# Kernel tuning notes

Measured on AMD Instinct MI355X. Metric: run time of the kernel, lower is better.

Reference implementation:

```python
import jax, jax.numpy as jnp
import numpy as np

N = 4096      # nodes
IN = 512      # in_features
HEADS = 8
HPH = 8       # n_hidden // n_heads
HID = HEADS * HPH  # 64
CLS = 16      # n_classes
NEG_SLOPE = 0.2
MASK_VAL = -1e9


def setup_inputs() -> dict:
    key = jax.random.key(0)
    ks = jax.random.split(key, 8)
    x = jax.random.normal(ks[0], (N, IN), jnp.float32)
    # sparse-ish adjacency, avg degree ~16, with self loops
    adj = jax.random.bernoulli(ks[1], 16.0 / N, (N, N)) | jnp.eye(N, dtype=bool)
    W1 = jax.random.normal(ks[2], (IN, HEADS, HPH), jnp.float32) * 0.05
    a1l = jax.random.normal(ks[3], (HEADS, HPH), jnp.float32) * 0.05
    a1r = jax.random.normal(ks[4], (HEADS, HPH), jnp.float32) * 0.05
    W2 = jax.random.normal(ks[5], (HID, 1, CLS), jnp.float32) * 0.05
    a2l = jax.random.normal(ks[6], (1, CLS), jnp.float32) * 0.05
    a2r = jax.random.normal(ks[7], (1, CLS), jnp.float32) * 0.05
    return {"x": x, "adj": adj, "W1": W1, "a1l": a1l, "a1r": a1r,
            "W2": W2, "a2l": a2l, "a2r": a2r}


def gat_layer(x, adj, W, al, ar, is_concat):
    # project: [N, H, D]
    g = jnp.einsum('ni,ihd->nhd', x, W)
    # score e[i,j,h] = leaky_relu(a_l . g_i + a_r . g_j)
    sl = jnp.einsum('nhd,hd->nh', g, al)  # [N, H]
    sr = jnp.einsum('nhd,hd->nh', g, ar)  # [N, H]
    e = jax.nn.leaky_relu(sl[:, None, :] + sr[None, :, :], NEG_SLOPE)  # [N, N, H]
    e = jnp.where(adj[:, :, None], e, MASK_VAL)
    a = jax.nn.softmax(e, axis=1)                 # softmax over neighbors j
    out = jnp.einsum('ijh,jhd->ihd', a, g)        # [N, H, D]
    if is_concat:
        return out.reshape(out.shape[0], -1)      # [N, H*D]
    return out.mean(axis=1)                        # [N, D]


def reference(x, adj, W1, a1l, a1r, W2, a2l, a2r):
    # dropout layers are identity in eval mode
    h = gat_layer(x, adj, W1, a1l, a1r, True)   # [N, HID]
    h = jax.nn.elu(h)
    return gat_layer(h, adj, W2, a2l, a2r, False)  # [N, CLS]
```

## Files before the change

kernel.cpp:

```cpp
#include <hip/hip_runtime.h>
#include <hip/hip_bf16.h>

#define N_NODES 4096
#define IN_F 512
#define HEADS 8
#define HPH 8
#define HID 64
#define CLS 16
#define NEG_SLOPE 0.2f
#define MAXD 256

__device__ __forceinline__ float leaky(float x) { return x > 0.f ? x : NEG_SLOPE * x; }

__global__ void proj1(const float* __restrict__ x,
                      const float* __restrict__ W1,
                      const float* __restrict__ a1l,
                      const float* __restrict__ a1r,
                      float* __restrict__ g1,
                      float* __restrict__ sl1,
                      float* __restrict__ sr1) {
    const int t  = threadIdx.x;
    const int nl = t >> 4;
    const int c4 = (t & 15) * 4;
    const int i0 = blockIdx.x * 16;
    __shared__ float xs[16][516];
    {
        const int row = nl;
        const float4* src = (const float4*)(x + (size_t)(i0 + row) * IN_F);
        float4* dst = (float4*)(&xs[row][0]);
        for (int k = (t & 15); k < IN_F / 4; k += 16) dst[k] = src[k];
    }
    __syncthreads();
    float4 acc = make_float4(0.f, 0.f, 0.f, 0.f);
    const float* xrow = &xs[nl][0];
#pragma unroll 4
    for (int k = 0; k < IN_F; k += 4) {
        const float4 xv = *(const float4*)(xrow + k);
        const float4 w0 = *(const float4*)(W1 + (size_t)(k + 0) * HID + c4);
        const float4 w1 = *(const float4*)(W1 + (size_t)(k + 1) * HID + c4);
        const float4 w2 = *(const float4*)(W1 + (size_t)(k + 2) * HID + c4);
        const float4 w3 = *(const float4*)(W1 + (size_t)(k + 3) * HID + c4);
        acc.x += xv.x * w0.x + xv.y * w1.x + xv.z * w2.x + xv.w * w3.x;
        acc.y += xv.x * w0.y + xv.y * w1.y + xv.z * w2.y + xv.w * w3.y;
        acc.z += xv.x * w0.z + xv.y * w1.z + xv.z * w2.z + xv.w * w3.z;
        acc.w += xv.x * w0.w + xv.y * w1.w + xv.z * w2.w + xv.w * w3.w;
    }
    const int i = i0 + nl;
    *(float4*)(g1 + (size_t)i * HID + c4) = acc;
    const float4 al = *(const float4*)(a1l + c4);
    const float4 ar = *(const float4*)(a1r + c4);
    float pl = acc.x * al.x + acc.y * al.y + acc.z * al.z + acc.w * al.w;
    float pr = acc.x * ar.x + acc.y * ar.y + acc.z * ar.z + acc.w * ar.w;
    pl += __shfl_xor(pl, 1, 64);
    pr += __shfl_xor(pr, 1, 64);
    if ((t & 1) == 0) {
        const int h = (t & 15) >> 1;
        sl1[i * HEADS + h] = pl;
        sr1[i * HEADS + h] = pr;
    }
}

__global__ void attn1_fused(const int* __restrict__ adj,
                            const float* __restrict__ g1,
                            const float* __restrict__ sl1,
                            const float* __restrict__ sr1,
                            const float* __restrict__ W2,
                            const float* __restrict__ a2l,
                            const float* __restrict__ a2r,
                            float* __restrict__ g2,
                            float* __restrict__ sl2,
                            float* __restrict__ sr2,
                            int* __restrict__ deg_g,
                            int* __restrict__ nbr_g) {
    const int i = blockIdx.x;
    const int t = threadIdx.x;
    __shared__ int nbr[MAXD];
    __shared__ int cnt;
    __shared__ float h1s[HID];
    if (t == 0) cnt = 0;
    __syncthreads();
    const int4* row = (const int4*)(adj + (size_t)i * N_NODES);
    for (int w = t; w < N_NODES / 4; w += 64) {
        int4 v = row[w];
        if (v.x | v.y | v.z | v.w) {
            if (v.x) { int p = atomicAdd(&cnt, 1); if (p < MAXD) nbr[p] = 4 * w + 0; }
            if (v.y) { int p = atomicAdd(&cnt, 1); if (p < MAXD) nbr[p] = 4 * w + 1; }
            if (v.z) { int p = atomicAdd(&cnt, 1); if (p < MAXD) nbr[p] = 4 * w + 2; }
            if (v.w) { int p = atomicAdd(&cnt, 1); if (p < MAXD) nbr[p] = 4 * w + 3; }
        }
    }
    __syncthreads();
    const int n = cnt < MAXD ? cnt : MAXD;
    if (t == 0) deg_g[i] = n;
    for (int k = t; k < n; k += 64) nbr_g[(size_t)i * MAXD + k] = nbr[k];

    const int h = t >> 3;
    const float sl = sl1[i * HEADS + h];
    float denom = 0.f, acc = 0.f;
    for (int k = 0; k < n; ++k) {
        const int jj = nbr[k];
        const float w = __expf(leaky(sl + sr1[jj * HEADS + h]));
        denom += w;
        acc += w * g1[(size_t)jj * HID + t];
    }
    float o = (n > 0) ? (acc / denom) : 0.f;
    o = (o > 0.f) ? o : expm1f(o);
    h1s[t] = o;
    __syncthreads();

    const int q = t >> 4, c = t & 15;
    float p = 0.f;
#pragma unroll
    for (int kk = 0; kk < 16; ++kk) {
        const int k2 = q * 16 + kk;
        p += h1s[k2] * W2[k2 * CLS + c];
    }
    p += __shfl_xor(p, 16, 64);
    p += __shfl_xor(p, 32, 64);
    float pl = 0.f, pr = 0.f;
    if (t < CLS) {
        g2[(size_t)i * CLS + t] = p;
        pl = p * a2l[t];
        pr = p * a2r[t];
    }
#pragma unroll
    for (int off = 1; off < 16; off <<= 1) {
        pl += __shfl_xor(pl, off, 64);
        pr += __shfl_xor(pr, off, 64);
    }
    if (t == 0) { sl2[i] = pl; sr2[i] = pr; }
}

__global__ void attn2(const int* __restrict__ deg_g,
                      const int* __restrict__ nbr_g,
                      const float* __restrict__ g2,
                      const float* __restrict__ sl2,
                      const float* __restrict__ sr2,
                      float* __restrict__ out) {
    const int t = threadIdx.x;
    const int g = t >> 4;
    const int c = t & 15;
    const int node = blockIdx.x * 4 + g;
    __shared__ int nbrs[4][MAXD];
    const int n = deg_g[node];
    for (int k = c; k < n; k += 16) nbrs[g][k] = nbr_g[(size_t)node * MAXD + k];
    __syncthreads();
    const float sl = sl2[node];
    float denom = 0.f, acc = 0.f;
    for (int k = 0; k < n; ++k) {
        const int jj = nbrs[g][k];
        const float w = __expf(leaky(sl + sr2[jj]));
        denom += w;
        acc += w * g2[(size_t)jj * CLS + c];
    }
    out[(size_t)node * CLS + c] = (n > 0) ? acc / denom : 0.f;
}

extern "C" void kernel_launch(void* const* d_in, const int* in_sizes, int n_in,
                              void* d_out, int out_size, void* d_ws, size_t ws_size,
                              hipStream_t stream) {
    const float* x   = (const float*)d_in[0];
    const int*   adj = (const int*)d_in[1];
    const float* W1  = (const float*)d_in[2];
    const float* a1l = (const float*)d_in[3];
    const float* a1r = (const float*)d_in[4];
    const float* W2  = (const float*)d_in[5];
    const float* a2l = (const float*)d_in[6];
    const float* a2r = (const float*)d_in[7];
    float* out = (float*)d_out;

    float* ws  = (float*)d_ws;
    float* g1  = ws;
    float* sl1 = g1  + (size_t)N_NODES * HID;
    float* sr1 = sl1 + (size_t)N_NODES * HEADS;
    float* g2  = sr1 + (size_t)N_NODES * HEADS;
    float* sl2 = g2  + (size_t)N_NODES * CLS;
    float* sr2 = sl2 + N_NODES;
    int*   deg = (int*)(sr2 + N_NODES);
    int*   nbr = deg + N_NODES;

    proj1<<<N_NODES / 16, 256, 0, stream>>>(x, W1, a1l, a1r, g1, sl1, sr1);
    attn1_fused<<<N_NODES, 64, 0, stream>>>(adj, g1, sl1, sr1, W2, a2l, a2r,
                                            g2, sl2, sr2, deg, nbr);
    attn2<<<N_NODES / 4, 64, 0, stream>>>(deg, nbr, g2, sl2, sr2, out);
}
```

Baseline: 151.8 us.

## Move adjacency scan into projection kernel and unroll neighbor aggregation loops

The per-row adjacency scan moves out of the attention kernel and into the projection kernel as extra 256-thread blocks, so the scan runs alongside the projection instead of serially inside a 64-thread attention block. The attention kernel now reads the compacted neighbor lists from global memory. Both aggregation loops are unrolled by four so several gathers are in flight at once. The cost is a larger first launch, extra global reads of the neighbor lists, and more registers per thread.

Result: slower. 172.1 us (+13.4%).

```diff
diff --git a/kernel.cpp b/kernel.cpp
--- a/kernel.cpp
+++ b/kernel.cpp
@@ -12,22 +12,48 @@
 
 __device__ __forceinline__ float leaky(float x) { return x > 0.f ? x : NEG_SLOPE * x; }
 
-__global__ void proj1(const float* __restrict__ x,
-                      const float* __restrict__ W1,
-                      const float* __restrict__ a1l,
-                      const float* __restrict__ a1r,
-                      float* __restrict__ g1,
-                      float* __restrict__ sl1,
-                      float* __restrict__ sr1) {
-    const int t  = threadIdx.x;
+__global__ __launch_bounds__(256) void scan_proj1(
+        const int* __restrict__ adj,
+        const float* __restrict__ x,
+        const float* __restrict__ W1,
+        const float* __restrict__ a1l,
+        const float* __restrict__ a1r,
+        float* __restrict__ g1,
+        float* __restrict__ sl1,
+        float* __restrict__ sr1,
+        int* __restrict__ deg_g,
+        int* __restrict__ nbr_g) {
+    __shared__ float xs[16][516];
+    const int b = blockIdx.x;
+    const int t = threadIdx.x;
+    if (b < N_NODES) {
+        int* nbrS = (int*)&xs[0][0];
+        __shared__ int cnt;
+        if (t == 0) cnt = 0;
+        __syncthreads();
+        const int4* row = (const int4*)(adj + (size_t)b * N_NODES);
+        for (int w = t; w < N_NODES / 4; w += 256) {
+            int4 v = row[w];
+            if (v.x | v.y | v.z | v.w) {
+                if (v.x) { int p = atomicAdd(&cnt, 1); if (p < MAXD) nbrS[p] = 4 * w + 0; }
+                if (v.y) { int p = atomicAdd(&cnt, 1); if (p < MAXD) nbrS[p] = 4 * w + 1; }
+                if (v.z) { int p = atomicAdd(&cnt, 1); if (p < MAXD) nbrS[p] = 4 * w + 2; }
+                if (v.w) { int p = atomicAdd(&cnt, 1); if (p < MAXD) nbrS[p] = 4 * w + 3; }
+            }
+        }
+        __syncthreads();
+        const int n = cnt < MAXD ? cnt : MAXD;
+        if (t == 0) deg_g[b] = n;
+        for (int k = t; k < n; k += 256) nbr_g[(size_t)b * MAXD + k] = nbrS[k];
+        return;
+    }
+    const int blk = b - N_NODES;
     const int nl = t >> 4;
     const int c4 = (t & 15) * 4;
-    const int i0 = blockIdx.x * 16;
-    __shared__ float xs[16][516];
+    const int i0 = blk * 16;
     {
-        const int row = nl;
-        const float4* src = (const float4*)(x + (size_t)(i0 + row) * IN_F);
-        float4* dst = (float4*)(&xs[row][0]);
+        const float4* src = (const float4*)(x + (size_t)(i0 + nl) * IN_F);
+        float4* dst = (float4*)(&xs[nl][0]);
         for (int k = (t & 15); k < IN_F / 4; k += 16) dst[k] = src[k];
     }
     __syncthreads();
@@ -60,44 +86,41 @@
     }
 }
 
-__global__ void attn1_fused(const int* __restrict__ adj,
-                            const float* __restrict__ g1,
-                            const float* __restrict__ sl1,
-                            const float* __restrict__ sr1,
-                            const float* __restrict__ W2,
-                            const float* __restrict__ a2l,
-                            const float* __restrict__ a2r,
-                            float* __restrict__ g2,
-                            float* __restrict__ sl2,
-                            float* __restrict__ sr2,
-                            int* __restrict__ deg_g,
-                            int* __restrict__ nbr_g) {
+__global__ __launch_bounds__(64) void attn1_fused(
+        const float* __restrict__ g1,
+        const float* __restrict__ sl1,
+        const float* __restrict__ sr1,
+        const float* __restrict__ W2,
+        const float* __restrict__ a2l,
+        const float* __restrict__ a2r,
+        const int* __restrict__ deg_g,
+        const int* __restrict__ nbr_g,
+        float* __restrict__ g2,
+        float* __restrict__ sl2,
+        float* __restrict__ sr2) {
     const int i = blockIdx.x;
     const int t = threadIdx.x;
     __shared__ int nbr[MAXD];
-    __shared__ int cnt;
     __shared__ float h1s[HID];
-    if (t == 0) cnt = 0;
-    __syncthreads();
-    const int4* row = (const int4*)(adj + (size_t)i * N_NODES);
-    for (int w = t; w < N_NODES / 4; w += 64) {
-        int4 v = row[w];
-        if (v.x | v.y | v.z | v.w) {
-            if (v.x) { int p = atomicAdd(&cnt, 1); if (p < MAXD) nbr[p] = 4 * w + 0; }
-            if (v.y) { int p = atomicAdd(&cnt, 1); if (p < MAXD) nbr[p] = 4 * w + 1; }
-            if (v.z) { int p = atomicAdd(&cnt, 1); if (p < MAXD) nbr[p] = 4 * w + 2; }
-            if (v.w) { int p = atomicAdd(&cnt, 1); if (p < MAXD) nbr[p] = 4 * w + 3; }
-        }
-    }
-    __syncthreads();
-    const int n = cnt < MAXD ? cnt : MAXD;
-    if (t == 0) deg_g[i] = n;
-    for (int k = t; k < n; k += 64) nbr_g[(size_t)i * MAXD + k] = nbr[k];
-
+    const int n = deg_g[i];
+    for (int k = t; k < n; k += 64) nbr[k] = nbr_g[(size_t)i * MAXD + k];
+    __syncthreads();
     const int h = t >> 3;
     const float sl = sl1[i * HEADS + h];
     float denom = 0.f, acc = 0.f;
-    for (int k = 0; k < n; ++k) {
+    int k = 0;
+    for (; k + 4 <= n; k += 4) {
+        const int j0 = nbr[k], j1 = nbr[k + 1], j2 = nbr[k + 2], j3 = nbr[k + 3];
+        const float s0 = sr1[j0 * HEADS + h], s1 = sr1[j1 * HEADS + h];
+        const float s2 = sr1[j2 * HEADS + h], s3 = sr1[j3 * HEADS + h];
+        const float v0 = g1[(size_t)j0 * HID + t], v1 = g1[(size_t)j1 * HID + t];
+        const float v2 = g1[(size_t)j2 * HID + t], v3 = g1[(size_t)j3 * HID + t];
+        const float w0 = __expf(leaky(sl + s0)), w1 = __expf(leaky(sl + s1));
+        const float w2 = __expf(leaky(sl + s2)), w3 = __expf(leaky(sl + s3));
+        denom += (w0 + w1) + (w2 + w3);
+        acc += w0 * v0; acc += w1 * v1; acc += w2 * v2; acc += w3 * v3;
+    }
+    for (; k < n; ++k) {
         const int jj = nbr[k];
         const float w = __expf(leaky(sl + sr1[jj * HEADS + h]));
         denom += w;
@@ -107,7 +130,6 @@
     o = (o > 0.f) ? o : expm1f(o);
     h1s[t] = o;
     __syncthreads();
-
     const int q = t >> 4, c = t & 15;
     float p = 0.f;
 #pragma unroll
@@ -131,12 +153,13 @@
     if (t == 0) { sl2[i] = pl; sr2[i] = pr; }
 }
 
-__global__ void attn2(const int* __restrict__ deg_g,
-                      const int* __restrict__ nbr_g,
-                      const float* __restrict__ g2,
-                      const float* __restrict__ sl2,
-                      const float* __restrict__ sr2,
-                      float* __restrict__ out) {
+__global__ __launch_bounds__(64) void attn2(
+        const int* __restrict__ deg_g,
+        const int* __restrict__ nbr_g,
+        const float* __restrict__ g2,
+        const float* __restrict__ sl2,
+        const float* __restrict__ sr2,
+        float* __restrict__ out) {
     const int t = threadIdx.x;
     const int g = t >> 4;
     const int c = t & 15;
@@ -147,7 +170,19 @@
     __syncthreads();
     const float sl = sl2[node];
     float denom = 0.f, acc = 0.f;
-    for (int k = 0; k < n; ++k) {
+    int k = 0;
+    for (; k + 4 <= n; k += 4) {
+        const int j0 = nbrs[g][k], j1 = nbrs[g][k + 1];
+        const int j2 = nbrs[g][k + 2], j3 = nbrs[g][k + 3];
+        const float s0 = sr2[j0], s1 = sr2[j1], s2 = sr2[j2], s3 = sr2[j3];
+        const float v0 = g2[(size_t)j0 * CLS + c], v1 = g2[(size_t)j1 * CLS + c];
+        const float v2 = g2[(size_t)j2 * CLS + c], v3 = g2[(size_t)j3 * CLS + c];
+        const float w0 = __expf(leaky(sl + s0)), w1 = __expf(leaky(sl + s1));
+        const float w2 = __expf(leaky(sl + s2)), w3 = __expf(leaky(sl + s3));
+        denom += (w0 + w1) + (w2 + w3);
+        acc += w0 * v0; acc += w1 * v1; acc += w2 * v2; acc += w3 * v3;
+    }
+    for (; k < n; ++k) {
         const int jj = nbrs[g][k];
         const float w = __expf(leaky(sl + sr2[jj]));
         denom += w;
@@ -179,8 +214,9 @@
     int*   deg = (int*)(sr2 + N_NODES);
     int*   nbr = deg + N_NODES;
 
-    proj1<<<N_NODES / 16, 256, 0, stream>>>(x, W1, a1l, a1r, g1, sl1, sr1);
-    attn1_fused<<<N_NODES, 64, 0, stream>>>(adj, g1, sl1, sr1, W2, a2l, a2r,
-                                            g2, sl2, sr2, deg, nbr);
+    scan_proj1<<<N_NODES + N_NODES / 16, 256, 0, stream>>>(
+        adj, x, W1, a1l, a1r, g1, sl1, sr1, deg, nbr);
+    attn1_fused<<<N_NODES, 64, 0, stream>>>(g1, sl1, sr1, W2, a2l, a2r,
+                                            deg, nbr, g2, sl2, sr2);
     attn2<<<N_NODES / 4, 64, 0, stream>>>(deg, nbr, g2, sl2, sr2, out);
 }
```
